# Kernel optimization log

Measured on AMD Instinct MI355X. Metric: run time of the kernel, lower is better.

The kernel has to match this reference:

```python
import jax, jax.numpy as jnp
import numpy as np

NUM_FORMULAS = 256
NUM_CONJ_ARR = [6, 9, 12, 15]
DEPTH_ARR = [2, 4, 6]
TEMPERATURE = 2.0
INPUT_DIM = 512
BATCH = 8192

# --- static DNF structure (mirrors build-time indicator matrices) ---
_group = NUM_FORMULAS // len(NUM_CONJ_ARR)                       # 64 formulas per group
_conj_per_formula = np.repeat(np.array(NUM_CONJ_ARR), _group)     # [F]
_CONJ2FORM = np.repeat(np.arange(NUM_FORMULAS), _conj_per_formula)  # [C] = 2688
TOTAL_CONJ = int(_CONJ2FORM.shape[0])
_depths = np.tile(np.array(DEPTH_ARR), TOTAL_CONJ // len(DEPTH_ARR))  # depth per conjunction
_LIT2CONJ = np.repeat(np.arange(TOTAL_CONJ), _depths)             # [L] = 10752
TOTAL_LIT = int(_LIT2CONJ.shape[0])


def setup_inputs() -> dict:
    key = jax.random.key(0)
    k = jax.random.split(key, 6)
    x = jax.random.normal(k[0], (BATCH, INPUT_DIM), jnp.float32)
    # literals_random_mask: binary feature-subset mask per literal (build-time constant)
    random_mask = (jax.random.uniform(k[1], (INPUT_DIM, TOTAL_LIT)) < 0.5).astype(jnp.float32)
    glorot = jnp.sqrt(2.0 / (INPUT_DIM + TOTAL_LIT))
    # weight is pre-multiplied by the random mask at build time
    weight = jax.random.normal(k[2], (INPUT_DIM, TOTAL_LIT), jnp.float32) * glorot * random_mask
    # learnable_binary_mask: soft binary-threshold output in [0, 1]
    learnable_binary_mask = jax.random.uniform(k[3], (INPUT_DIM, TOTAL_LIT), jnp.float32)
    bias = jnp.zeros((TOTAL_LIT,), jnp.float32)
    mu = jax.random.normal(k[4], (NUM_FORMULAS, INPUT_DIM), jnp.float32)
    sigma = 1.0 + 0.1 * jax.random.uniform(k[5], (NUM_FORMULAS,), jnp.float32)
    return {
        "x": x, "weight": weight, "learnable_binary_mask": learnable_binary_mask,
        "bias": bias, "mu": mu, "sigma": sigma,
        "lit2conj": jnp.asarray(_LIT2CONJ, jnp.int32),
        "conj2form": jnp.asarray(_CONJ2FORM, jnp.int32),
    }


def reference(x, weight, learnable_binary_mask, bias, mu, sigma, lit2conj, conj2form):
    # literal projection: tanh(x @ (W * M) + b)             -> [B, L]
    literals = jnp.tanh(x @ (weight * learnable_binary_mask) + bias)
    # soft AND over literals of each conjunction: tanh(sum - d + 1.5)
    and_bias = jax.ops.segment_sum(jnp.ones((TOTAL_LIT,), literals.dtype), lit2conj,
                                   num_segments=TOTAL_CONJ)
    conj_sum = jax.ops.segment_sum(literals.T, lit2conj, num_segments=TOTAL_CONJ).T  # [B, C]
    conj = jnp.tanh(conj_sum - and_bias + 1.5)
    # soft OR over conjunctions of each formula: tanh(sum + d - 1.5)
    or_bias = jax.ops.segment_sum(jnp.ones((TOTAL_CONJ,), conj.dtype), conj2form,
                                  num_segments=NUM_FORMULAS)
    form_sum = jax.ops.segment_sum(conj.T, conj2form, num_segments=NUM_FORMULAS).T   # [B, F]
    dnnf = jnp.tanh(form_sum + or_bias - 1.5)
    # localization: softmax over formulas of temperature-scaled RBF, via GEMM expansion
    sq = (jnp.sum(x * x, axis=1, keepdims=True) - 2.0 * (x @ mu.T)
          + jnp.sum(mu * mu, axis=1)[None, :])                                       # [B, F]
    loc = jax.nn.softmax(TEMPERATURE * jnp.exp(-0.5 * sq / (sigma * sigma)[None, :]), axis=-1)
    return dnnf * loc
```

## Files before the change

### kernel.cpp

```cpp
#include <hip/hip_runtime.h>


#define BATCH 8192
#define IDIM 512
#define NFORM 256
#define NLIT 10752
#define WT_ROWS 11136

#define BM 128
#define BN 192
#define BK 64
#define BUFB 40960
#define SLITP 196

typedef __bf16 bf16x8 __attribute__((ext_vector_type(8)));
typedef float f32x4 __attribute__((ext_vector_type(4)));
typedef unsigned short u16;
typedef unsigned int u32;

__device__ __forceinline__ u16 f2bf(float f) {
  u32 u = __float_as_uint(f);
  u = (u + 0x7fffu + ((u >> 16) & 1u)) >> 16;
  return (u16)u;
}

__device__ __forceinline__ float fast_tanh(float x) {
  float e = __expf(2.0f * x);
  return 1.0f - 2.0f * __builtin_amdgcn_rcpf(e + 1.0f);
}

__device__ __forceinline__ void async_cp16(const void* g, void* l) {
  __builtin_amdgcn_global_load_lds(
      (const u32 __attribute__((address_space(1)))*)g,
      (u32 __attribute__((address_space(3)))*)l, 16, 0, 0);
}


#define PREPX_BLKS 2048
#define PREPW_BLKS 1344

__global__ __launch_bounds__(256) void prep_all(
    const float* __restrict__ x, const float* __restrict__ W,
    const float* __restrict__ M, const float* __restrict__ mu,
    u16* __restrict__ xb, u16* __restrict__ wt, float* __restrict__ xsq,
    float* __restrict__ musq, float* __restrict__ form_sum) {
  __shared__ float lds[64 * 65];
  const int blk = blockIdx.x, tid = threadIdx.x;

  if (blk < PREPX_BLKS) {
    ((uint4*)form_sum)[blk * 256 + tid] = make_uint4(0, 0, 0, 0);
    int wave = tid >> 6, lane = tid & 63;
    int row = blk * 4 + wave;
    const float4* px = (const float4*)(x + (size_t)row * IDIM);
    float4 a = px[lane * 2], b = px[lane * 2 + 1];
    uint4 pk;
    pk.x = (u32)f2bf(a.x) | ((u32)f2bf(a.y) << 16);
    pk.y = (u32)f2bf(a.z) | ((u32)f2bf(a.w) << 16);
    pk.z = (u32)f2bf(b.x) | ((u32)f2bf(b.y) << 16);
    pk.w = (u32)f2bf(b.z) | ((u32)f2bf(b.w) << 16);
    ((uint4*)(xb + (size_t)row * IDIM))[lane] = pk;
    float s = a.x * a.x + a.y * a.y + a.z * a.z + a.w * a.w +
              b.x * b.x + b.y * b.y + b.z * b.z + b.w * b.w;
#pragma unroll
    for (int o = 32; o > 0; o >>= 1) s += __shfl_down(s, o);
    if (lane == 0) xsq[row] = s;
  } else if (blk < PREPX_BLKS + PREPW_BLKS) {
    int b = blk - PREPX_BLKS;
    int l0 = (b % 168) * 64, k0 = (b / 168) * 64;
#pragma unroll
    for (int j = 0; j < 4; ++j) {
      int idx = tid + j * 256;
      int kk = idx >> 4, l4 = idx & 15;
      size_t g = (size_t)(k0 + kk) * NLIT + l0 + l4 * 4;
      float4 w4 = *(const float4*)(W + g);
      float4 m4 = *(const float4*)(M + g);
      lds[kk * 65 + l4 * 4 + 0] = w4.x * m4.x;
      lds[kk * 65 + l4 * 4 + 1] = w4.y * m4.y;
      lds[kk * 65 + l4 * 4 + 2] = w4.z * m4.z;
      lds[kk * 65 + l4 * 4 + 3] = w4.w * m4.w;
    }
    __syncthreads();
    int l = tid >> 2, kq = tid & 3;
    u32 pk[8];
#pragma unroll
    for (int t = 0; t < 8; ++t) {
      u16 lo = f2bf(lds[(kq * 16 + 2 * t) * 65 + l]);
      u16 hi = f2bf(lds[(kq * 16 + 2 * t + 1) * 65 + l]);
      pk[t] = (u32)lo | ((u32)hi << 16);
    }
    u32* dst = (u32*)(wt + (size_t)(l0 + l) * IDIM + k0 + kq * 16);
    ((uint4*)dst)[0] = make_uint4(pk[0], pk[1], pk[2], pk[3]);
    ((uint4*)dst)[1] = make_uint4(pk[4], pk[5], pk[6], pk[7]);
  } else {
    int b = blk - PREPX_BLKS - PREPW_BLKS;
    if (b < 256) {
      float s = 0.f;
#pragma unroll
      for (int j = tid; j < IDIM; j += 256) {
        float v = mu[(size_t)b * IDIM + j];
        wt[(size_t)(NLIT + b) * IDIM + j] = f2bf(v);
        s += v * v;
      }
      float* red = lds;
      red[tid] = s;
      __syncthreads();
      for (int sh = 128; sh > 0; sh >>= 1) {
        if (tid < sh) red[tid] += red[tid + sh];
        __syncthreads();
      }
      if (tid == 0) musq[b] = red[0];
    } else {
      int row = NLIT + 256 + (b - 256);
      for (int j = tid; j < IDIM; j += 256) wt[(size_t)row * IDIM + j] = 0;
    }
  }
}


__global__ __launch_bounds__(256, 2) void dnnf_gemm(
    const u16* __restrict__ xb, const u16* __restrict__ wt,
    const float* __restrict__ bias, float* __restrict__ form_sum,
    float* __restrict__ dotbuf) {
  __shared__ __align__(16) char smraw[2 * BUFB];
  float* slit = (float*)smraw;

  const int tid = threadIdx.x;
  const int wave = tid >> 6, lane = tid & 63;
  const int wm = wave & 1, wn = wave >> 1;
  const int m0 = blockIdx.x * BM, n0 = blockIdx.y * BN;
  const int q = lane >> 4, cn = lane & 15;

  const int kg8 = ((tid & 7) ^ ((tid >> 3) & 7)) * 8;
  const u16* pa = xb + (size_t)(m0 + (tid >> 3)) * IDIM + kg8;
  const u16* pb = wt + (size_t)(n0 + (tid >> 3)) * IDIM + kg8;
  const int dA = tid * 16;
  const int dB = 16384 + tid * 16;

  const int kg0_16 = ((q ^ (cn & 7)) << 4);
  int offA[4], offB[6];
#pragma unroll
  for (int mf = 0; mf < 4; ++mf)
    offA[mf] = (wm * 64 + mf * 16 + cn) * 128 + kg0_16;
#pragma unroll
  for (int nf = 0; nf < 6; ++nf)
    offB[nf] = 16384 + (wn * 96 + nf * 16 + cn) * 128 + kg0_16;

  f32x4 acc[4][6];
#pragma unroll
  for (int a = 0; a < 4; ++a)
#pragma unroll
    for (int b = 0; b < 6; ++b) acc[a][b] = (f32x4){0.f, 0.f, 0.f, 0.f};

#pragma unroll
  for (int i = 0; i < 4; ++i)
    async_cp16(pa + (size_t)i * 32 * IDIM, smraw + dA + i * 4096);
#pragma unroll
  for (int i = 0; i < 6; ++i)
    async_cp16(pb + (size_t)i * 32 * IDIM, smraw + dB + i * 4096);
  pa += BK;
  pb += BK;

#pragma unroll
  for (int kt = 0; kt < 8; ++kt) {
    const char* bufc = smraw + (kt & 1) * BUFB;
    if (kt < 7) {
      char* bufn = smraw + ((kt + 1) & 1) * BUFB;
#pragma unroll
      for (int i = 0; i < 4; ++i)
        async_cp16(pa + (size_t)i * 32 * IDIM, bufn + dA + i * 4096);
#pragma unroll
      for (int i = 0; i < 6; ++i)
        async_cp16(pb + (size_t)i * 32 * IDIM, bufn + dB + i * 4096);
      pa += BK;
      pb += BK;
      asm volatile("s_waitcnt vmcnt(10)\n\ts_barrier" ::: "memory");
    } else {
      asm volatile("s_waitcnt vmcnt(0)\n\ts_barrier" ::: "memory");
    }
#pragma unroll
    for (int ks = 0; ks < 2; ++ks) {
      const int x64 = ks ? 64 : 0;
      bf16x8 af[4], bfr[6];
#pragma unroll
      for (int mf = 0; mf < 4; ++mf)
        af[mf] = *(const bf16x8*)(bufc + (offA[mf] ^ x64));
#pragma unroll
      for (int nf = 0; nf < 6; ++nf)
        bfr[nf] = *(const bf16x8*)(bufc + (offB[nf] ^ x64));
#pragma unroll
      for (int mf = 0; mf < 4; ++mf)
#pragma unroll
        for (int nf = 0; nf < 6; ++nf)
          acc[mf][nf] = __builtin_amdgcn_mfma_f32_16x16x32_bf16(
              af[mf], bfr[nf], acc[mf][nf], 0, 0, 0);
    }
    if (kt < 7)
      asm volatile("s_waitcnt lgkmcnt(0)\n\ts_barrier" ::: "memory");
  }
  __syncthreads();

  if (n0 < NLIT) {
    float bv[6];
#pragma unroll
    for (int nf = 0; nf < 6; ++nf) bv[nf] = bias[n0 + wn * 96 + nf * 16 + cn];

#pragma unroll
    for (int ph = 0; ph < 2; ++ph) {
      if (ph) __syncthreads();
      if (wm == ph) {
#pragma unroll
        for (int nf = 0; nf < 6; ++nf) {
          int col = wn * 96 + nf * 16 + cn;
#pragma unroll
          for (int mf = 0; mf < 4; ++mf)
#pragma unroll
            for (int reg = 0; reg < 4; ++reg) {
              int lr = mf * 16 + q * 4 + reg;
              slit[lr * SLITP + col] = fast_tanh(acc[mf][nf][reg] + bv[nf]);
            }
        }
      }
      __syncthreads();

      int r = tid >> 2, sub = tid & 3;
      const float* lrow = slit + r * SLITP + sub * 48;
      int c0 = ((n0 + sub * 48) / 12) * 3;
      size_t grow = (size_t)(m0 + ph * 64 + r) * NFORM;
      float run = 0.f;
      int fprev = -1;
#pragma unroll
      for (int tr = 0; tr < 4; ++tr) {
        const float* p = lrow + tr * 12;
        float s2 = p[0] + p[1];
        float s4 = p[2] + p[3] + p[4] + p[5];
        float s6 = p[6] + p[7] + p[8] + p[9] + p[10] + p[11];
        float v = fast_tanh(s2 - 0.5f) + fast_tanh(s4 - 2.5f) +
                  fast_tanh(s6 - 4.5f);
        int c = c0 + tr * 3;
        int f = (c < 384)    ? (c / 6)
                : (c < 960)  ? 64 + (c - 384) / 9
                : (c < 1728) ? 128 + (c - 960) / 12
                             : 192 + (c - 1728) / 15;
        if (f != fprev) {
          if (fprev >= 0) atomicAdd(form_sum + grow + fprev, run);
          fprev = f;
          run = 0.f;
        }
        run += v;
      }
      atomicAdd(form_sum + grow + fprev, run);
    }
  } else {
#pragma unroll
    for (int nf = 0; nf < 6; ++nf) {
      int col = n0 - NLIT + wn * 96 + nf * 16 + cn;
      if (col < NFORM) {
#pragma unroll
        for (int mf = 0; mf < 4; ++mf)
#pragma unroll
          for (int reg = 0; reg < 4; ++reg) {
            int row = wm * 64 + mf * 16 + q * 4 + reg;
            dotbuf[(size_t)(m0 + row) * NFORM + col] = acc[mf][nf][reg];
          }
      }
    }
  }
}


__global__ __launch_bounds__(256) void finale(
    const float* __restrict__ form_sum, const float* __restrict__ dotbuf,
    const float* __restrict__ xsq, const float* __restrict__ musq,
    const float* __restrict__ sigma, float* __restrict__ out) {
  int wave = threadIdx.x >> 6, lane = threadIdx.x & 63;
  int r = blockIdx.x * 4 + wave;
  size_t base = (size_t)r * NFORM;
  float xs = xsq[r];
  float e[4], s = 0.f;
#pragma unroll
  for (int j = 0; j < 4; ++j) {
    int f = j * 64 + lane;
    float sq = xs - 2.0f * dotbuf[base + f] + musq[f];
    float sg = sigma[f];
    float p = __expf(-0.5f * sq / (sg * sg));
    e[j] = __expf(2.0f * p);
    s += e[j];
  }
#pragma unroll
  for (int o = 32; o > 0; o >>= 1) s += __shfl_xor(s, o);
  float inv = __builtin_amdgcn_rcpf(s);
#pragma unroll
  for (int j = 0; j < 4; ++j) {
    int f = j * 64 + lane;
    float dn = fast_tanh(form_sum[base + f] + (float)(6 + 3 * j) - 1.5f);
    out[base + f] = dn * e[j] * inv;
  }
}


extern "C" void kernel_launch(void* const* d_in, const int* in_sizes, int n_in,
                              void* d_out, int out_size, void* d_ws,
                              size_t ws_size, hipStream_t stream) {
  const float* x = (const float*)d_in[0];
  const float* W = (const float*)d_in[1];
  const float* M = (const float*)d_in[2];
  const float* bias = (const float*)d_in[3];
  const float* mu = (const float*)d_in[4];
  const float* sigma = (const float*)d_in[5];
  float* out = (float*)d_out;

  float* form_sum = (float*)d_ws;
  float* dotbuf = form_sum + (size_t)BATCH * NFORM;
  u16* xb = (u16*)(dotbuf + (size_t)BATCH * NFORM);
  u16* wt = xb + (size_t)BATCH * IDIM;
  float* xsq = (float*)(wt + (size_t)WT_ROWS * IDIM);
  float* musq = xsq + BATCH;

  prep_all<<<PREPX_BLKS + PREPW_BLKS + 384, 256, 0, stream>>>(
      x, W, M, mu, xb, wt, xsq, musq, form_sum);
  dnnf_gemm<<<dim3(BATCH / BM, WT_ROWS / BN), 256, 0, stream>>>(xb, wt, bias,
                                                                form_sum, dotbuf);
  finale<<<BATCH / 4, 256, 0, stream>>>(form_sum, dotbuf, xsq, musq, sigma, out);
}
```

Baseline: 234.0 us.

## Load A fragments directly from global into registers to shrink LDS and raise occupancy

The x (A) tile is no longer staged through shared memory. Each wave loads its A fragments straight from global memory into registers every k-step, and only the W tile is double-buffered in LDS. The LDS buffer drops from 40 KB to 24 KB per stage and launch bounds rise to three blocks per CU. The epilogue is split into four 32-row passes so its literal staging fits the smaller shared buffer. In exchange, A loads are uncoalesced per-lane 16-byte reads that are repeated across the waves sharing rows, and register pressure rises under the tighter launch bound.

After: 295.6 us. +26.3%, slower.

```diff
diff --git a/kernel.cpp b/kernel.cpp
--- a/kernel.cpp
+++ b/kernel.cpp
@@ -10,7 +10,7 @@
 #define BM 128
 #define BN 192
 #define BK 64
-#define BUFB 40960
+#define BUFB 24576
 #define SLITP 196
 
 typedef __bf16 bf16x8 __attribute__((ext_vector_type(8)));
@@ -117,7 +117,7 @@
 }
 
 
-__global__ __launch_bounds__(256, 2) void dnnf_gemm(
+__global__ __launch_bounds__(256, 3) void dnnf_gemm(
     const u16* __restrict__ xb, const u16* __restrict__ wt,
     const float* __restrict__ bias, float* __restrict__ form_sum,
     float* __restrict__ dotbuf) {
@@ -131,19 +131,16 @@
   const int q = lane >> 4, cn = lane & 15;
 
   const int kg8 = ((tid & 7) ^ ((tid >> 3) & 7)) * 8;
-  const u16* pa = xb + (size_t)(m0 + (tid >> 3)) * IDIM + kg8;
   const u16* pb = wt + (size_t)(n0 + (tid >> 3)) * IDIM + kg8;
-  const int dA = tid * 16;
-  const int dB = 16384 + tid * 16;
+  const int dB = tid * 16;
+
+  const u16* pA = xb + (size_t)(m0 + wm * 64 + cn) * IDIM + q * 8;
 
   const int kg0_16 = ((q ^ (cn & 7)) << 4);
-  int offA[4], offB[6];
-#pragma unroll
-  for (int mf = 0; mf < 4; ++mf)
-    offA[mf] = (wm * 64 + mf * 16 + cn) * 128 + kg0_16;
+  int offB[6];
 #pragma unroll
   for (int nf = 0; nf < 6; ++nf)
-    offB[nf] = 16384 + (wn * 96 + nf * 16 + cn) * 128 + kg0_16;
+    offB[nf] = (wn * 96 + nf * 16 + cn) * 128 + kg0_16;
 
   f32x4 acc[4][6];
 #pragma unroll
@@ -151,39 +148,35 @@
 #pragma unroll
     for (int b = 0; b < 6; ++b) acc[a][b] = (f32x4){0.f, 0.f, 0.f, 0.f};
 
-#pragma unroll
-  for (int i = 0; i < 4; ++i)
-    async_cp16(pa + (size_t)i * 32 * IDIM, smraw + dA + i * 4096);
 #pragma unroll
   for (int i = 0; i < 6; ++i)
     async_cp16(pb + (size_t)i * 32 * IDIM, smraw + dB + i * 4096);
-  pa += BK;
   pb += BK;
 
 #pragma unroll
   for (int kt = 0; kt < 8; ++kt) {
     const char* bufc = smraw + (kt & 1) * BUFB;
+    bf16x8 af[2][4];
+#pragma unroll
+    for (int ks = 0; ks < 2; ++ks)
+#pragma unroll
+      for (int mf = 0; mf < 4; ++mf)
+        af[ks][mf] = *(const bf16x8*)(pA + (size_t)mf * 16 * IDIM +
+                                      kt * BK + ks * 32);
     if (kt < 7) {
       char* bufn = smraw + ((kt + 1) & 1) * BUFB;
 #pragma unroll
-      for (int i = 0; i < 4; ++i)
-        async_cp16(pa + (size_t)i * 32 * IDIM, bufn + dA + i * 4096);
-#pragma unroll
       for (int i = 0; i < 6; ++i)
         async_cp16(pb + (size_t)i * 32 * IDIM, bufn + dB + i * 4096);
-      pa += BK;
       pb += BK;
-      asm volatile("s_waitcnt vmcnt(10)\n\ts_barrier" ::: "memory");
+      asm volatile("s_waitcnt vmcnt(14)\n\ts_barrier" ::: "memory");
     } else {
-      asm volatile("s_waitcnt vmcnt(0)\n\ts_barrier" ::: "memory");
+      asm volatile("s_waitcnt vmcnt(8)\n\ts_barrier" ::: "memory");
     }
 #pragma unroll
     for (int ks = 0; ks < 2; ++ks) {
       const int x64 = ks ? 64 : 0;
-      bf16x8 af[4], bfr[6];
-#pragma unroll
-      for (int mf = 0; mf < 4; ++mf)
-        af[mf] = *(const bf16x8*)(bufc + (offA[mf] ^ x64));
+      bf16x8 bfr[6];
 #pragma unroll
       for (int nf = 0; nf < 6; ++nf)
         bfr[nf] = *(const bf16x8*)(bufc + (offB[nf] ^ x64));
@@ -192,7 +185,7 @@
 #pragma unroll
         for (int nf = 0; nf < 6; ++nf)
           acc[mf][nf] = __builtin_amdgcn_mfma_f32_16x16x32_bf16(
-              af[mf], bfr[nf], acc[mf][nf], 0, 0, 0);
+              af[ks][mf], bfr[nf], acc[mf][nf], 0, 0, 0);
     }
     if (kt < 7)
       asm volatile("s_waitcnt lgkmcnt(0)\n\ts_barrier" ::: "memory");
@@ -205,35 +198,37 @@
     for (int nf = 0; nf < 6; ++nf) bv[nf] = bias[n0 + wn * 96 + nf * 16 + cn];
 
 #pragma unroll
-    for (int ph = 0; ph < 2; ++ph) {
-      if (ph) __syncthreads();
-      if (wm == ph) {
-#pragma unroll
-        for (int nf = 0; nf < 6; ++nf) {
-          int col = wn * 96 + nf * 16 + cn;
-#pragma unroll
-          for (int mf = 0; mf < 4; ++mf)
+    for (int p = 0; p < 4; ++p) {
+      if (p) __syncthreads();
+      if (wm == (p >> 1)) {
+#pragma unroll
+        for (int mh = 0; mh < 2; ++mh) {
+          int mf = 2 * (p & 1) + mh;
+#pragma unroll
+          for (int nf = 0; nf < 6; ++nf) {
+            int col = wn * 96 + nf * 16 + cn;
 #pragma unroll
             for (int reg = 0; reg < 4; ++reg) {
-              int lr = mf * 16 + q * 4 + reg;
+              int lr = mh * 16 + q * 4 + reg;
               slit[lr * SLITP + col] = fast_tanh(acc[mf][nf][reg] + bv[nf]);
             }
+          }
         }
       }
       __syncthreads();
 
-      int r = tid >> 2, sub = tid & 3;
-      const float* lrow = slit + r * SLITP + sub * 48;
-      int c0 = ((n0 + sub * 48) / 12) * 3;
-      size_t grow = (size_t)(m0 + ph * 64 + r) * NFORM;
+      int r = tid >> 3, sub = tid & 7;
+      const float* lrow = slit + r * SLITP + sub * 24;
+      int c0 = ((n0 + sub * 24) / 12) * 3;
+      size_t grow = (size_t)(m0 + p * 32 + r) * NFORM;
       float run = 0.f;
       int fprev = -1;
 #pragma unroll
-      for (int tr = 0; tr < 4; ++tr) {
-        const float* p = lrow + tr * 12;
-        float s2 = p[0] + p[1];
-        float s4 = p[2] + p[3] + p[4] + p[5];
-        float s6 = p[6] + p[7] + p[8] + p[9] + p[10] + p[11];
+      for (int tr = 0; tr < 2; ++tr) {
+        const float* pp = lrow + tr * 12;
+        float s2 = pp[0] + pp[1];
+        float s4 = pp[2] + pp[3] + pp[4] + pp[5];
+        float s6 = pp[6] + pp[7] + pp[8] + pp[9] + pp[10] + pp[11];
         float v = fast_tanh(s2 - 0.5f) + fast_tanh(s4 - 2.5f) +
                   fast_tanh(s6 - 4.5f);
         int c = c0 + tr * 3;
```

## Switch GEMM mainloop to three-stage pipeline with BK=32 and new swizzle

Applied to the files above, without the earlier changes.

Replaces the double-buffered BK=64 main loop with a three-stage ring of BK=32 tiles, prefetching two stages ahead and adjusting vmcnt waits. The LDS swizzle is redesigned for 64-byte rows. Shared memory falls from 80 KB to 60 KB, which may let more blocks fit per CU, and deeper prefetch aims to hide global latency. In exchange there are twice as many barriers and each k-step carries fewer MFMAs per sync.

Measured after the change: 245.8 us. 5.0% more time.

```diff
diff --git a/kernel.cpp b/kernel.cpp
--- a/kernel.cpp
+++ b/kernel.cpp
@@ -9,8 +9,8 @@
 
 #define BM 128
 #define BN 192
-#define BK 64
-#define BUFB 40960
+#define BK 32
+#define STAGEB 20480
 #define SLITP 196
 
 typedef __bf16 bf16x8 __attribute__((ext_vector_type(8)));
@@ -121,7 +121,7 @@
     const u16* __restrict__ xb, const u16* __restrict__ wt,
     const float* __restrict__ bias, float* __restrict__ form_sum,
     float* __restrict__ dotbuf) {
-  __shared__ __align__(16) char smraw[2 * BUFB];
+  __shared__ __align__(16) char smraw[3 * STAGEB];
   float* slit = (float*)smraw;
 
   const int tid = threadIdx.x;
@@ -130,20 +130,36 @@
   const int m0 = blockIdx.x * BM, n0 = blockIdx.y * BN;
   const int q = lane >> 4, cn = lane & 15;
 
-  const int kg8 = ((tid & 7) ^ ((tid >> 3) & 7)) * 8;
-  const u16* pa = xb + (size_t)(m0 + (tid >> 3)) * IDIM + kg8;
-  const u16* pb = wt + (size_t)(n0 + (tid >> 3)) * IDIM + kg8;
-  const int dA = tid * 16;
-  const int dB = 16384 + tid * 16;
-
-  const int kg0_16 = ((q ^ (cn & 7)) << 4);
+  const u16* sp[5];
+  int dofs[5];
+#pragma unroll
+  for (int i = 0; i < 5; ++i) {
+    int c = tid + i * 256;
+    dofs[i] = c * 16;
+    if (i < 2) {
+      int r = c >> 2;
+      int kg = (c & 3) ^ (r & 3) ^ ((r >> 2) & 3);
+      sp[i] = xb + (size_t)(m0 + r) * IDIM + kg * 8;
+    } else {
+      int r = (c - 512) >> 2;
+      int kg = (c & 3) ^ (r & 3) ^ ((r >> 2) & 3);
+      sp[i] = wt + (size_t)(n0 + r) * IDIM + kg * 8;
+    }
+  }
+
   int offA[4], offB[6];
 #pragma unroll
-  for (int mf = 0; mf < 4; ++mf)
-    offA[mf] = (wm * 64 + mf * 16 + cn) * 128 + kg0_16;
-#pragma unroll
-  for (int nf = 0; nf < 6; ++nf)
-    offB[nf] = 16384 + (wn * 96 + nf * 16 + cn) * 128 + kg0_16;
+  for (int mf = 0; mf < 4; ++mf) {
+    int row = wm * 64 + mf * 16 + cn;
+    int f = (row & 3) ^ ((row >> 2) & 3);
+    offA[mf] = row * 64 + ((q ^ f) << 4);
+  }
+#pragma unroll
+  for (int nf = 0; nf < 6; ++nf) {
+    int row = wn * 96 + nf * 16 + cn;
+    int f = (row & 3) ^ ((row >> 2) & 3);
+    offB[nf] = 8192 + row * 64 + ((q ^ f) << 4);
+  }
 
   f32x4 acc[4][6];
 #pragma unroll
@@ -152,50 +168,41 @@
     for (int b = 0; b < 6; ++b) acc[a][b] = (f32x4){0.f, 0.f, 0.f, 0.f};
 
 #pragma unroll
-  for (int i = 0; i < 4; ++i)
-    async_cp16(pa + (size_t)i * 32 * IDIM, smraw + dA + i * 4096);
-#pragma unroll
-  for (int i = 0; i < 6; ++i)
-    async_cp16(pb + (size_t)i * 32 * IDIM, smraw + dB + i * 4096);
-  pa += BK;
-  pb += BK;
-
-#pragma unroll
-  for (int kt = 0; kt < 8; ++kt) {
-    const char* bufc = smraw + (kt & 1) * BUFB;
-    if (kt < 7) {
-      char* bufn = smraw + ((kt + 1) & 1) * BUFB;
-#pragma unroll
-      for (int i = 0; i < 4; ++i)
-        async_cp16(pa + (size_t)i * 32 * IDIM, bufn + dA + i * 4096);
-#pragma unroll
-      for (int i = 0; i < 6; ++i)
-        async_cp16(pb + (size_t)i * 32 * IDIM, bufn + dB + i * 4096);
-      pa += BK;
-      pb += BK;
+  for (int s = 0; s < 2; ++s)
+#pragma unroll
+    for (int i = 0; i < 5; ++i)
+      async_cp16(sp[i] + s * BK, smraw + s * STAGEB + dofs[i]);
+
+#pragma unroll
+  for (int kt = 0; kt < 16; ++kt) {
+    const char* bufc = smraw + (kt % 3) * STAGEB;
+    if (kt > 0) {
+      asm volatile("s_waitcnt lgkmcnt(0)\n\ts_barrier" ::: "memory");
+    }
+    if (kt < 14) {
+      char* bufn = smraw + ((kt + 2) % 3) * STAGEB;
+#pragma unroll
+      for (int i = 0; i < 5; ++i)
+        async_cp16(sp[i] + (kt + 2) * BK, bufn + dofs[i]);
       asm volatile("s_waitcnt vmcnt(10)\n\ts_barrier" ::: "memory");
+    } else if (kt == 14) {
+      asm volatile("s_waitcnt vmcnt(5)\n\ts_barrier" ::: "memory");
     } else {
       asm volatile("s_waitcnt vmcnt(0)\n\ts_barrier" ::: "memory");
     }
-#pragma unroll
-    for (int ks = 0; ks < 2; ++ks) {
-      const int x64 = ks ? 64 : 0;
-      bf16x8 af[4], bfr[6];
-#pragma unroll
-      for (int mf = 0; mf < 4; ++mf)
-        af[mf] = *(const bf16x8*)(bufc + (offA[mf] ^ x64));
+    bf16x8 af[4], bfr[6];
+#pragma unroll
+    for (int mf = 0; mf < 4; ++mf)
+      af[mf] = *(const bf16x8*)(bufc + offA[mf]);
+#pragma unroll
+    for (int nf = 0; nf < 6; ++nf)
+      bfr[nf] = *(const bf16x8*)(bufc + offB[nf]);
+#pragma unroll
+    for (int mf = 0; mf < 4; ++mf)
 #pragma unroll
       for (int nf = 0; nf < 6; ++nf)
-        bfr[nf] = *(const bf16x8*)(bufc + (offB[nf] ^ x64));
-#pragma unroll
-      for (int mf = 0; mf < 4; ++mf)
-#pragma unroll
-        for (int nf = 0; nf < 6; ++nf)
-          acc[mf][nf] = __builtin_amdgcn_mfma_f32_16x16x32_bf16(
-              af[mf], bfr[nf], acc[mf][nf], 0, 0, 0);
-    }
-    if (kt < 7)
-      asm volatile("s_waitcnt lgkmcnt(0)\n\ts_barrier" ::: "memory");
+        acc[mf][nf] = __builtin_amdgcn_mfma_f32_16x16x32_bf16(
+            af[mf], bfr[nf], acc[mf][nf], 0, 0, 0);
   }
   __syncthreads();
 
```
